# Kernel tuning notes

Measured on AMD Instinct MI355X. Metric: run time of the kernel, lower is better.

## Reference

```python
import jax, jax.numpy as jnp
import numpy as np


def _apply_rope(x, rope):
    # x: (B, T, D); rope: (T, D//2, 2) broadcast over batch
    B, T, D = x.shape
    x_ = x.reshape(B, T, D // 2, 2)
    cos, sin = rope[..., 0], rope[..., 1]
    xr, xi = x_[..., 0], x_[..., 1]
    rotr = xr * cos - xi * sin
    roti = xr * sin + xi * cos
    return jnp.stack([rotr, roti], axis=-1).reshape(B, T, D)


def setup_inputs() -> dict:
    key = jax.random.key(0)
    k1, k2, k3, k4 = jax.random.split(key, 4)
    B, T, D, H = 2, 2048, 1024, 16
    x = jax.random.normal(k1, (B, T, D), dtype=jnp.float32)
    rope = jax.random.normal(k2, (T, D // 2, 2), dtype=jnp.float32)
    w_qkv = jax.random.normal(k3, (3 * D, D), dtype=jnp.float32) * (1.0 / np.sqrt(D))
    w_proj = jax.random.normal(k4, (D, D), dtype=jnp.float32) * (1.0 / np.sqrt(D))
    return {"x": x, "rope": rope, "w_qkv": w_qkv, "w_proj": w_proj}


def reference(x, rope, w_qkv, w_proj):
    B, T, D = x.shape
    H = 16
    dk = D // H
    qkv = jnp.einsum("btd,ed->bte", x, w_qkv)  # (B, T, 3D)
    q, k, v = jnp.split(qkv, 3, axis=-1)
    q = _apply_rope(q, rope)
    k = _apply_rope(k, rope)
    # split heads: (B, H, T, dk)
    q = q.reshape(B, T, H, dk).transpose(0, 2, 1, 3)
    k = k.reshape(B, T, H, dk).transpose(0, 2, 1, 3)
    v = v.reshape(B, T, H, dk).transpose(0, 2, 1, 3)
    att = jnp.einsum("bhqd,bhkd->bhqk", q, k) / jnp.sqrt(jnp.float32(dk)).astype(x.dtype)
    att = jax.nn.softmax(att, axis=-1)
    out = jnp.einsum("bhqk,bhkd->bhqd", att, v)
    out = out.transpose(0, 2, 1, 3).reshape(B, T, D)
    return jnp.einsum("btd,ed->bte", out, w_proj)
```

## Files before the change

kernel.cpp:

```cpp
#include <hip/hip_runtime.h>

typedef _Float16 f16;
typedef _Float16 f16x2 __attribute__((ext_vector_type(2)));
typedef _Float16 f16x4 __attribute__((ext_vector_type(4)));
typedef _Float16 f16x8 __attribute__((ext_vector_type(8)));
typedef float    f32x2 __attribute__((ext_vector_type(2)));
typedef float    f32x4 __attribute__((ext_vector_type(4)));
typedef short    s16x4 __attribute__((ext_vector_type(4)));

#define GLDS16(gptr, lptr)                                                     \
  __builtin_amdgcn_global_load_lds(                                            \
      (const __attribute__((address_space(1))) void*)(gptr),                   \
      (__attribute__((address_space(3))) void*)(lptr), 16, 0, 0)

#define S_BARRIER() __builtin_amdgcn_s_barrier()
#define FENCE() asm volatile("" ::: "memory")
#define WAIT_VM8() asm volatile("s_waitcnt vmcnt(8)" ::: "memory")
#define WAIT_VM0() asm volatile("s_waitcnt vmcnt(0)" ::: "memory")
#define WAIT_LGKM0() asm volatile("s_waitcnt lgkmcnt(0)" ::: "memory")

__device__ inline short f32_to_bf16_rne(float f) {
  unsigned u = __builtin_bit_cast(unsigned, f);
  return (short)((u + 0x7FFFu + ((u >> 16) & 1u)) >> 16);
}

__global__ __launch_bounds__(256) void k_cast3(const float* __restrict__ a,
                                               const float* __restrict__ b,
                                               const float* __restrict__ c,
                                               f16* __restrict__ oa,
                                               f16* __restrict__ ob,
                                               f16* __restrict__ oc) {
  int i = blockIdx.x * 256 + threadIdx.x;
  const float* src;
  f16* dst;
  int off;
  if (i < 1048576) { src = a; dst = oa; off = i; }
  else if (i < 1835008) { src = b; dst = ob; off = i - 1048576; }
  else { src = c; dst = oc; off = i - 1835008; }
  f32x4 v = ((const f32x4*)src)[off];
  f16x4 h;
  h[0] = (f16)v[0]; h[1] = (f16)v[1]; h[2] = (f16)v[2]; h[3] = (f16)v[3];
  ((f16x4*)dst)[off] = h;
}

__global__ __launch_bounds__(256, 4) void k_gemm_qkv(
    const f16* __restrict__ A, const f16* __restrict__ B,
    const float* __restrict__ rope, f16* __restrict__ qh,
    f16* __restrict__ kh, short* __restrict__ vt) {
  const int K = 1024;
  __shared__ f16 sA[128 * 64];
  __shared__ f16 sB[128 * 64];
  const int tid = threadIdx.x;
  const int wave = tid >> 6, lane = tid & 63;
  const int lr = lane & 15, lq = lane >> 4;
  const int lr7 = lr & 7;
  const int wm = (wave >> 1) * 64, wn = (wave & 1) * 64;
  const size_t m0 = (size_t)blockIdx.x * 128, n0 = (size_t)blockIdx.y * 128;

  f32x4 acc[4][4] = {};

  const int sw8 = ((tid & 7) ^ ((tid >> 3) & 7)) * 8;
  const f16* ga = A + (m0 + (tid >> 3)) * (size_t)K + sw8;
  const f16* gb = B + (n0 + (tid >> 3)) * (size_t)K + sw8;

  for (int k0 = 0; k0 < K; k0 += 64) {
    __syncthreads();
#pragma unroll
    for (int r = 0; r < 4; ++r) {
      GLDS16(ga + (size_t)(r * 32) * K + k0, (char*)sA + r * 4096 + wave * 1024);
      GLDS16(gb + (size_t)(r * 32) * K + k0, (char*)sB + r * 4096 + wave * 1024);
    }
    __syncthreads();

#pragma unroll
    for (int kk = 0; kk < 2; ++kk) {
      f16x8 af[4], bf[4];
#pragma unroll
      for (int i = 0; i < 4; ++i)
        af[i] = *(const f16x8*)&sA[(wm + i * 16 + lr) * 64 +
                                   (((kk * 4 + lq) ^ lr7) * 8)];
#pragma unroll
      for (int j = 0; j < 4; ++j)
        bf[j] = *(const f16x8*)&sB[(wn + j * 16 + lr) * 64 +
                                   (((kk * 4 + lq) ^ lr7) * 8)];
#pragma unroll
      for (int i = 0; i < 4; ++i)
#pragma unroll
        for (int j = 0; j < 4; ++j)
          acc[i][j] = __builtin_amdgcn_mfma_f32_16x16x32_f16(af[i], bf[j],
                                                             acc[i][j], 0, 0, 0);
    }
  }

  const int region = (int)(n0 >> 10);
  if (region == 2) {
#pragma unroll
    for (int i = 0; i < 4; ++i)
#pragma unroll
      for (int j = 0; j < 4; ++j) {
        int e = (int)(n0 + wn + j * 16 + lr) - 2048;
        int h = e >> 6, c = e & 63;
        int m = (int)(m0 + wm + i * 16 + lq * 4);
        int b = m >> 11, t0 = m & 2047;
        s16x4 o;
#pragma unroll
        for (int r = 0; r < 4; ++r) o[r] = f32_to_bf16_rne(acc[i][j][r]);
        *(s16x4*)&vt[(((size_t)(b * 16 + h)) * 64 + c) * 2048 + t0] = o;
      }
  } else {
    const float scl = region == 0 ? 0.1803368801111204f : 1.0f;
    f16* dst = region == 0 ? qh : kh;
    const int odd = lr & 1;
#pragma unroll
    for (int i = 0; i < 4; ++i)
#pragma unroll
      for (int j = 0; j < 4; ++j) {
        int e = ((int)(n0 + wn + j * 16 + lr)) & 1023;
        int h = e >> 6, c = e & 63, p = e >> 1;
        int mb = (int)(m0 + wm + i * 16 + lq * 4);
        int b = mb >> 11;
#pragma unroll
        for (int r = 0; r < 4; ++r) {
          int t = (mb + r) & 2047;
          float v = acc[i][j][r];
          float partner = __shfl_xor(v, 1);
          f32x2 cs = *(const f32x2*)&rope[((size_t)t * 512 + p) * 2];
          float out = odd ? (partner * cs[1] + v * cs[0])
                          : (v * cs[0] - partner * cs[1]);
          dst[(((size_t)(b * 16 + h)) * 2048 + t) * 64 + c] = (f16)(out * scl);
        }
      }
  }
}

__global__ __launch_bounds__(256, 4) void k_gemm_bt64(const f16* __restrict__ A,
                                                      const f16* __restrict__ B,
                                                      float* __restrict__ C,
                                                      int M, int N, int K) {
  __shared__ f16 sA[128 * 64];
  __shared__ f16 sB[64 * 64];
  const int tid = threadIdx.x;
  const int wave = tid >> 6, lane = tid & 63;
  const int lr = lane & 15, lq = lane >> 4;
  const int lr7 = lr & 7;
  const int wm = wave * 32;
  const size_t m0 = (size_t)blockIdx.x * 128, n0 = (size_t)blockIdx.y * 64;

  f32x4 acc[2][4] = {};

  const int sw8 = ((tid & 7) ^ ((tid >> 3) & 7)) * 8;
  const f16* ga = A + (m0 + (tid >> 3)) * (size_t)K + sw8;
  const f16* gb = B + (n0 + (tid >> 3)) * (size_t)K + sw8;

  for (int k0 = 0; k0 < K; k0 += 64) {
    __syncthreads();
#pragma unroll
    for (int r = 0; r < 4; ++r)
      GLDS16(ga + (size_t)(r * 32) * K + k0, (char*)sA + r * 4096 + wave * 1024);
#pragma unroll
    for (int r = 0; r < 2; ++r)
      GLDS16(gb + (size_t)(r * 32) * K + k0, (char*)sB + r * 4096 + wave * 1024);
    __syncthreads();

#pragma unroll
    for (int kk = 0; kk < 2; ++kk) {
      f16x8 af[2], bf[4];
#pragma unroll
      for (int i = 0; i < 2; ++i)
        af[i] = *(const f16x8*)&sA[(wm + i * 16 + lr) * 64 +
                                   (((kk * 4 + lq) ^ lr7) * 8)];
#pragma unroll
      for (int j = 0; j < 4; ++j)
        bf[j] = *(const f16x8*)&sB[(j * 16 + lr) * 64 +
                                   (((kk * 4 + lq) ^ lr7) * 8)];
#pragma unroll
      for (int i = 0; i < 2; ++i)
#pragma unroll
        for (int j = 0; j < 4; ++j)
          acc[i][j] = __builtin_amdgcn_mfma_f32_16x16x32_f16(af[i], bf[j],
                                                             acc[i][j], 0, 0, 0);
    }
  }

#pragma unroll
  for (int i = 0; i < 2; ++i)
#pragma unroll
    for (int j = 0; j < 4; ++j)
#pragma unroll
      for (int r = 0; r < 4; ++r)
        C[(m0 + wm + i * 16 + lq * 4 + r) * (size_t)N + n0 + j * 16 + lr] =
            acc[i][j][r];
}

__global__ __launch_bounds__(256, 2) void k_attn(const f16* __restrict__ Qp,
                                                 const f16* __restrict__ Kp,
                                                 const short* __restrict__ Vt,
                                                 f16* __restrict__ Op) {
  __shared__ f16 sQ[128 * 64];
  __shared__ f16 sKV[2 * 16384];
  const int tid = threadIdx.x, wave = tid >> 6, lane = tid & 63;
  const int lr = lane & 15, lq = lane >> 4;
  const int lr7 = lr & 7;
  const int bh = blockIdx.x, qt = blockIdx.y;
  const size_t base = (size_t)bh * 2048 * 64;

  const int sw8 = ((tid & 7) ^ ((tid >> 3) & 7)) * 8;
  const int sw16 = ((tid & 15) ^ ((tid >> 4) & 15)) * 8;

  auto stage_kv = [&](int jcc, int d) {
    const f16* gk = Kp + base + (size_t)jcc * 128 * 64;
    const short* gv = Vt + base + (size_t)jcc * 128;
    char* bK = (char*)sKV + d * 32768;
    char* bV = bK + 16384;
#pragma unroll
    for (int r = 0; r < 4; ++r) {
      GLDS16(gk + (size_t)(r * 32 + (tid >> 3)) * 64 + sw8,
             bK + r * 4096 + wave * 1024);
      GLDS16(gv + (size_t)(r * 16 + (tid >> 4)) * 2048 + sw16,
             bV + r * 4096 + wave * 1024);
    }
  };

  const f16* gq = Qp + base + (size_t)qt * 128 * 64;
#pragma unroll
  for (int r = 0; r < 4; ++r)
    GLDS16(gq + (size_t)(r * 32 + (tid >> 3)) * 64 + sw8,
           (char*)sQ + r * 4096 + wave * 1024);
  stage_kv(0, 0);
  WAIT_VM8();
  S_BARRIER();
  FENCE();
  f16x8 qa0 = *(const f16x8*)&sQ[(wave * 32 + lr) * 64 + ((lq ^ lr7) * 8)];
  f16x8 qa1 = *(const f16x8*)&sQ[(wave * 32 + lr) * 64 + (((4 + lq) ^ lr7) * 8)];
  f16x8 qb0 = *(const f16x8*)&sQ[(wave * 32 + 16 + lr) * 64 + ((lq ^ lr7) * 8)];
  f16x8 qb1 =
      *(const f16x8*)&sQ[(wave * 32 + 16 + lr) * 64 + (((4 + lq) ^ lr7) * 8)];

  f32x4 ota[4] = {}, otb[4] = {};
  f32x4 la4 = {}, lb4 = {};
  const s16x4 ones = {(short)0x3F80, (short)0x3F80, (short)0x3F80,
                      (short)0x3F80};

#pragma unroll 1
  for (int jc = 0; jc < 16; ++jc) {
    const int cur = jc & 1;
    if (jc < 15) {
      stage_kv(jc + 1, cur ^ 1);
      WAIT_VM8();
    } else {
      WAIT_VM0();
    }
    S_BARRIER();
    FENCE();

    const f16* bK = (const f16*)((char*)sKV + cur * 32768);
    const short* bV = (const short*)((char*)sKV + cur * 32768 + 16384);

    s16x4 pfa[8], pfb[8];
#pragma unroll
    for (int nt = 0; nt < 8; ++nt) {
      f16x8 kf0 = *(const f16x8*)&bK[(nt * 16 + lr) * 64 + ((lq ^ lr7) * 8)];
      f16x8 kf1 =
          *(const f16x8*)&bK[(nt * 16 + lr) * 64 + (((4 + lq) ^ lr7) * 8)];
      f32x4 z = {0.f, 0.f, 0.f, 0.f};
      f32x4 sa = __builtin_amdgcn_mfma_f32_16x16x32_f16(kf0, qa0, z, 0, 0, 0);
      sa = __builtin_amdgcn_mfma_f32_16x16x32_f16(kf1, qa1, sa, 0, 0, 0);
      f32x4 sb = __builtin_amdgcn_mfma_f32_16x16x32_f16(kf0, qb0, z, 0, 0, 0);
      sb = __builtin_amdgcn_mfma_f32_16x16x32_f16(kf1, qb1, sb, 0, 0, 0);
#pragma unroll
      for (int r = 0; r < 4; ++r) {
        float pa = __builtin_amdgcn_exp2f(sa[r]);
        float pb = __builtin_amdgcn_exp2f(sb[r]);
        pfa[nt][r] = (short)(__builtin_bit_cast(unsigned, pa) >> 16);
        pfb[nt][r] = (short)(__builtin_bit_cast(unsigned, pb) >> 16);
      }
    }

#pragma unroll
    for (int ks = 0; ks < 8; ++ks) {
      la4 = __builtin_amdgcn_mfma_f32_16x16x16bf16_1k(ones, pfa[ks], la4,
                                                      0, 0, 0);
      lb4 = __builtin_amdgcn_mfma_f32_16x16x16bf16_1k(ones, pfb[ks], lb4,
                                                      0, 0, 0);
    }

#pragma unroll
    for (int d = 0; d < 4; ++d)
#pragma unroll
      for (int ks = 0; ks < 8; ++ks) {
        int vslot = (ks * 2 + (lq >> 1)) ^ lr;
        s16x4 vf = *(const s16x4*)&bV[(d * 16 + lr) * 128 + vslot * 8 +
                                      (lq & 1) * 4];
        ota[d] = __builtin_amdgcn_mfma_f32_16x16x16bf16_1k(vf, pfa[ks], ota[d],
                                                           0, 0, 0);
        otb[d] = __builtin_amdgcn_mfma_f32_16x16x16bf16_1k(vf, pfb[ks], otb[d],
                                                           0, 0, 0);
      }

    WAIT_LGKM0();
    S_BARRIER();
    FENCE();
  }

  float rla = 1.f / la4[0], rlb = 1.f / lb4[0];
  int b = bh >> 4, h = bh & 15;
  int ta = qt * 128 + wave * 32 + lr;
  f16* gouta = Op + ((size_t)(b * 2048 + ta)) * 1024 + h * 64;
  f16* goutb = gouta + (size_t)16 * 1024;
#pragma unroll
  for (int d = 0; d < 4; ++d) {
    f16x4 oa, ob;
#pragma unroll
    for (int r = 0; r < 4; ++r) {
      oa[r] = (f16)(ota[d][r] * rla);
      ob[r] = (f16)(otb[d][r] * rlb);
    }
    *(f16x4*)&gouta[d * 16 + lq * 4] = oa;
    *(f16x4*)&goutb[d * 16 + lq * 4] = ob;
  }
}

extern "C" void kernel_launch(void* const* d_in, const int* in_sizes, int n_in,
                              void* d_out, int out_size, void* d_ws,
                              size_t ws_size, hipStream_t stream) {
  const float* x     = (const float*)d_in[0];
  const float* rope  = (const float*)d_in[1];
  const float* wqkv  = (const float*)d_in[2];
  const float* wproj = (const float*)d_in[3];
  float* out = (float*)d_out;

  char* w = (char*)d_ws;
  const size_t MB = 1024 * 1024;
  f16* xh   = (f16*)(w + 0);
  f16* wqh  = (f16*)(w + 8 * MB);
  f16* wph  = (f16*)(w + 14 * MB);
  f16* qh   = (f16*)(w + 16 * MB);
  f16* kh   = (f16*)(w + 24 * MB);
  short* vth = (short*)(w + 32 * MB);
  f16* aoh  = (f16*)(w + 40 * MB);

  k_cast3<<<8192, 256, 0, stream>>>(x, wqkv, wproj, xh, wqh, wph);

  k_gemm_qkv<<<dim3(32, 24), 256, 0, stream>>>(xh, wqh, rope, qh, kh, vth);

  k_attn<<<dim3(32, 16), 256, 0, stream>>>(qh, kh, vth, aoh);

  k_gemm_bt64<<<dim3(32, 16), 256, 0, stream>>>(aoh, wph, out, 4096, 1024,
                                                1024);
}
```

Measured before the change: 190.9 us.

## Enlarge output-projection GEMM tile to 128x128 and compute softmax row sums in registers

The output projection GEMM moves from 128x64 to 128x128 tiles with a 2x2 wave layout, each wave holding a 64x64 accumulator, which halves the grid and raises data reuse per LDS load. In attention, the softmax denominator was accumulated with extra MFMAs against a ones vector; it is now summed in fp32 registers and reduced across lanes with shuffles at the end. The trade-offs are higher register pressure in the GEMM, fewer blocks for the GPU's many CUs, and a denominator taken from unrounded fp32 probabilities rather than their bf16-truncated values.

```diff
diff --git a/kernel.cpp b/kernel.cpp
--- a/kernel.cpp
+++ b/kernel.cpp
@@ -133,20 +133,20 @@
   }
 }
 
-__global__ __launch_bounds__(256, 4) void k_gemm_bt64(const f16* __restrict__ A,
-                                                      const f16* __restrict__ B,
-                                                      float* __restrict__ C,
-                                                      int M, int N, int K) {
+__global__ __launch_bounds__(256, 4) void k_gemm_bt(const f16* __restrict__ A,
+                                                    const f16* __restrict__ B,
+                                                    float* __restrict__ C,
+                                                    int M, int N, int K) {
   __shared__ f16 sA[128 * 64];
-  __shared__ f16 sB[64 * 64];
+  __shared__ f16 sB[128 * 64];
   const int tid = threadIdx.x;
   const int wave = tid >> 6, lane = tid & 63;
   const int lr = lane & 15, lq = lane >> 4;
   const int lr7 = lr & 7;
-  const int wm = wave * 32;
-  const size_t m0 = (size_t)blockIdx.x * 128, n0 = (size_t)blockIdx.y * 64;
-
-  f32x4 acc[2][4] = {};
+  const int wm = (wave >> 1) * 64, wn = (wave & 1) * 64;
+  const size_t m0 = (size_t)blockIdx.x * 128, n0 = (size_t)blockIdx.y * 128;
+
+  f32x4 acc[4][4] = {};
 
   const int sw8 = ((tid & 7) ^ ((tid >> 3) & 7)) * 8;
   const f16* ga = A + (m0 + (tid >> 3)) * (size_t)K + sw8;
@@ -155,26 +155,25 @@
   for (int k0 = 0; k0 < K; k0 += 64) {
     __syncthreads();
 #pragma unroll
-    for (int r = 0; r < 4; ++r)
+    for (int r = 0; r < 4; ++r) {
       GLDS16(ga + (size_t)(r * 32) * K + k0, (char*)sA + r * 4096 + wave * 1024);
-#pragma unroll
-    for (int r = 0; r < 2; ++r)
       GLDS16(gb + (size_t)(r * 32) * K + k0, (char*)sB + r * 4096 + wave * 1024);
+    }
     __syncthreads();
 
 #pragma unroll
     for (int kk = 0; kk < 2; ++kk) {
-      f16x8 af[2], bf[4];
-#pragma unroll
-      for (int i = 0; i < 2; ++i)
+      f16x8 af[4], bf[4];
+#pragma unroll
+      for (int i = 0; i < 4; ++i)
         af[i] = *(const f16x8*)&sA[(wm + i * 16 + lr) * 64 +
                                    (((kk * 4 + lq) ^ lr7) * 8)];
 #pragma unroll
       for (int j = 0; j < 4; ++j)
-        bf[j] = *(const f16x8*)&sB[(j * 16 + lr) * 64 +
+        bf[j] = *(const f16x8*)&sB[(wn + j * 16 + lr) * 64 +
                                    (((kk * 4 + lq) ^ lr7) * 8)];
 #pragma unroll
-      for (int i = 0; i < 2; ++i)
+      for (int i = 0; i < 4; ++i)
 #pragma unroll
         for (int j = 0; j < 4; ++j)
           acc[i][j] = __builtin_amdgcn_mfma_f32_16x16x32_f16(af[i], bf[j],
@@ -183,12 +182,12 @@
   }
 
 #pragma unroll
-  for (int i = 0; i < 2; ++i)
+  for (int i = 0; i < 4; ++i)
 #pragma unroll
     for (int j = 0; j < 4; ++j)
 #pragma unroll
       for (int r = 0; r < 4; ++r)
-        C[(m0 + wm + i * 16 + lq * 4 + r) * (size_t)N + n0 + j * 16 + lr] =
+        C[(m0 + wm + i * 16 + lq * 4 + r) * (size_t)N + n0 + wn + j * 16 + lr] =
             acc[i][j][r];
 }
 
@@ -237,9 +236,7 @@
       *(const f16x8*)&sQ[(wave * 32 + 16 + lr) * 64 + (((4 + lq) ^ lr7) * 8)];
 
   f32x4 ota[4] = {}, otb[4] = {};
-  f32x4 la4 = {}, lb4 = {};
-  const s16x4 ones = {(short)0x3F80, (short)0x3F80, (short)0x3F80,
-                      (short)0x3F80};
+  float la = 0.f, lb = 0.f;
 
 #pragma unroll 1
   for (int jc = 0; jc < 16; ++jc) {
@@ -271,17 +268,10 @@
       for (int r = 0; r < 4; ++r) {
         float pa = __builtin_amdgcn_exp2f(sa[r]);
         float pb = __builtin_amdgcn_exp2f(sb[r]);
+        la += pa; lb += pb;
         pfa[nt][r] = (short)(__builtin_bit_cast(unsigned, pa) >> 16);
         pfb[nt][r] = (short)(__builtin_bit_cast(unsigned, pb) >> 16);
       }
-    }
-
-#pragma unroll
-    for (int ks = 0; ks < 8; ++ks) {
-      la4 = __builtin_amdgcn_mfma_f32_16x16x16bf16_1k(ones, pfa[ks], la4,
-                                                      0, 0, 0);
-      lb4 = __builtin_amdgcn_mfma_f32_16x16x16bf16_1k(ones, pfb[ks], lb4,
-                                                      0, 0, 0);
     }
 
 #pragma unroll
@@ -302,7 +292,9 @@
     FENCE();
   }
 
-  float rla = 1.f / la4[0], rlb = 1.f / lb4[0];
+  la += __shfl_xor(la, 16); la += __shfl_xor(la, 32);
+  lb += __shfl_xor(lb, 16); lb += __shfl_xor(lb, 32);
+  float rla = 1.f / la, rlb = 1.f / lb;
   int b = bh >> 4, h = bh & 15;
   int ta = qt * 128 + wave * 32 + lr;
   f16* gouta = Op + ((size_t)(b * 2048 + ta)) * 1024 + h * 64;
@@ -345,6 +337,5 @@
 
   k_attn<<<dim3(32, 16), 256, 0, stream>>>(qh, kh, vth, aoh);
 
-  k_gemm_bt64<<<dim3(32, 16), 256, 0, stream>>>(aoh, wph, out, 4096, 1024,
-                                                1024);
-}
+  k_gemm_bt<<<dim3(32, 8), 256, 0, stream>>>(aoh, wph, out, 4096, 1024, 1024);
+}
```

Measured after the change: 181.8 us. 1.05x faster.
